# Kernel tuning notes

Hardware: AMD Instinct MI355X
Metric: run time of the kernel (lower is better)

The kernel has to match this reference:

```python
import jax, jax.numpy as jnp
import numpy as np

B, T, D = 2, 2048, 1024
NH, NKV, HD = 16, 4, 64
KD = NKV * HD          # 256
PD = 16                # rope partial dim (rotated dims)
RANK = 8
ALPHA = 1.0
ROPE_BASE = 10000.0


def setup_inputs() -> dict:
    key = jax.random.key(0)
    ks = jax.random.split(key, 10)
    s = 0.02
    return {
        "x":      jax.random.normal(ks[0], (B, T, D), jnp.float32),
        "Wq":     jax.random.normal(ks[1], (D, D), jnp.float32) * s,
        "Wk":     jax.random.normal(ks[2], (KD, D), jnp.float32) * s,
        "Wv":     jax.random.normal(ks[3], (KD, D), jnp.float32) * s,
        "Wproj":  jax.random.normal(ks[4], (D, D), jnp.float32) * s,
        "q_gain": jnp.full((NH,), 5.25, jnp.float32),
        "Aq":     jax.random.normal(ks[5], (RANK, D), jnp.float32) * s,
        "Bq":     jax.random.normal(ks[6], (D, RANK), jnp.float32) * s,
        "Av":     jax.random.normal(ks[7], (RANK, D), jnp.float32) * s,
        "Bv":     jax.random.normal(ks[8], (KD, RANK), jnp.float32) * s,
    }


def _rms_norm(x):
    # F.rms_norm with no weight: x / sqrt(mean(x^2) + eps), eps = dtype machine eps
    eps = jnp.finfo(x.dtype).eps
    return x * jax.lax.rsqrt(jnp.mean(x * x, axis=-1, keepdims=True) + eps)


def _rope_partial(x, cos, sin, pd):
    # x: [B, T, H, HD]; rotate first pd dims (half/half), pass rest through
    h = pd // 2
    x1, x2, rest = x[..., :h], x[..., h:pd], x[..., pd:]
    c = cos[None, :, None, :]  # [1, T, 1, h]
    s = sin[None, :, None, :]
    return jnp.concatenate([x1 * c + x2 * s, -x2 * c + x1 * s, rest], axis=-1)


def reference(x, Wq, Wk, Wv, Wproj, q_gain, Aq, Bq, Av, Bv):
    # projections + per-step LoRA on Q and V (output = alpha * B(A(x)))
    q = x @ Wq.T + ALPHA * ((x @ Aq.T) @ Bq.T)          # [B,T,D]
    k = x @ Wk.T                                        # [B,T,KD]
    v = x @ Wv.T + ALPHA * ((x @ Av.T) @ Bv.T)          # [B,T,KD]

    q = _rms_norm(q.reshape(B, T, NH, HD))
    k = _rms_norm(k.reshape(B, T, NKV, HD))
    v = v.reshape(B, T, NKV, HD)

    # partial RoPE tables: [T, PD//2]
    inv = 1.0 / (ROPE_BASE ** (jnp.arange(0, PD, 2, dtype=jnp.float32) / PD))
    freqs = jnp.arange(T, dtype=jnp.float32)[:, None] * inv[None, :]
    cos, sin = jnp.cos(freqs), jnp.sin(freqs)
    q = _rope_partial(q, cos, sin, PD)
    k = _rope_partial(k, cos, sin, PD)

    # learned per-head QK gain on queries
    q = q * q_gain[None, None, :, None]

    # GQA: repeat-interleave kv heads to NH
    g = NH // NKV
    kf = jnp.repeat(k, g, axis=2)  # [B,T,NH,HD]
    vf = jnp.repeat(v, g, axis=2)

    scale = 1.0 / np.float32(np.sqrt(HD))
    scores = jnp.einsum('bqhd,bkhd->bhqk', q, kf) * scale  # [B,NH,T,T]
    causal = jnp.tril(jnp.ones((T, T), bool))
    scores = jnp.where(causal[None, None], scores, -jnp.inf)
    p = jax.nn.softmax(scores, axis=-1)
    y = jnp.einsum('bhqk,bkhd->bqhd', p, vf).reshape(B, T, D)
    return y @ Wproj.T
```

## Files before the change

### kernel.cpp

```cpp
#include <hip/hip_runtime.h>

#define Tn   2048
#define Dn   1024
#define KDn  256
#define NHn  16
#define NKVn 4
#define Rn   4096

typedef short bf16x8 __attribute__((ext_vector_type(8)));
typedef float f32x4  __attribute__((ext_vector_type(4)));
typedef const __attribute__((address_space(1))) unsigned* gas_p;
typedef __attribute__((address_space(3))) unsigned* las_p;

__device__ unsigned short g_q[(size_t)Rn * Dn];
__device__ unsigned short g_k[(size_t)Rn * KDn];
__device__ unsigned short g_vt[(size_t)2 * NKVn * 64 * Tn];
__device__ unsigned short g_y[(size_t)Rn * Dn];
__device__ unsigned short g_xb[(size_t)Rn * Dn];
__device__ unsigned short g_wq[(size_t)Dn * Dn];
__device__ unsigned short g_wk[(size_t)KDn * Dn];
__device__ unsigned short g_wv[(size_t)KDn * Dn];
__device__ unsigned short g_wp[(size_t)Dn * Dn];
__device__ float g_tq[Rn * 8];
__device__ float g_tv[Rn * 8];

static __device__ __forceinline__ float bf2f(unsigned short u) {
    return __uint_as_float(((unsigned)u) << 16);
}
static __device__ __forceinline__ unsigned short f2bf(float f) {
    unsigned u = __float_as_uint(f);
    u += 0x7fffu + ((u >> 16) & 1u);
    return (unsigned short)(u >> 16);
}
static __device__ __forceinline__ unsigned pk2bf(float a, float b) {
    return (unsigned)f2bf(a) | ((unsigned)f2bf(b) << 16);
}
static __device__ __forceinline__ unsigned cvtpk(float a, float b) {
    unsigned r;
    asm("v_cvt_pk_bf16_f32 %0, %1, %2" : "=v"(r) : "v"(a), "v"(b));
    return r;
}
static __device__ __forceinline__ float wave_sum(float s) {
    #pragma unroll
    for (int off = 32; off; off >>= 1) s += __shfl_xor(s, off);
    return s;
}

__global__ __launch_bounds__(256)
void lora_tmp(const float* __restrict__ x,
              const float* __restrict__ Aq,
              const float* __restrict__ Av) {
    int tid = threadIdx.x, wave = tid >> 6, lane = tid & 63;
    int row = blockIdx.x * 4 + wave;
    const float2* xr = (const float2*)(x + (size_t)row * Dn);
    unsigned* xbo = (unsigned*)g_xb + (size_t)row * (Dn / 2);
    float aq[8], av[8];
    #pragma unroll
    for (int r = 0; r < 8; r++) { aq[r] = 0.f; av[r] = 0.f; }
    for (int it = 0; it < Dn / 128; it++) {
        int j = it * 64 + lane;
        float2 xv = xr[j];
        xbo[j] = pk2bf(xv.x, xv.y);
        #pragma unroll
        for (int r = 0; r < 8; r++) {
            float2 a2 = ((const float2*)(Aq + (size_t)r * Dn))[j];
            aq[r] += xv.x * a2.x + xv.y * a2.y;
        }
        #pragma unroll
        for (int r = 0; r < 8; r++) {
            float2 a2 = ((const float2*)(Av + (size_t)r * Dn))[j];
            av[r] += xv.x * a2.x + xv.y * a2.y;
        }
    }
    #pragma unroll
    for (int r = 0; r < 8; r++) { aq[r] = wave_sum(aq[r]); av[r] = wave_sum(av[r]); }
    if (lane == 0) {
        #pragma unroll
        for (int r = 0; r < 8; r++) { g_tq[row * 8 + r] = aq[r]; g_tv[row * 8 + r] = av[r]; }
    }
}

#define NQ4 (Dn * Dn / 4)
#define NK4 (KDn * Dn / 4)
__global__ __launch_bounds__(256)
void cast_w(const float* __restrict__ Wq, const float* __restrict__ Wk,
            const float* __restrict__ Wv, const float* __restrict__ Wp) {
    int i = blockIdx.x * 256 + threadIdx.x;
    const float* src; unsigned short* dst; int o;
    if      (i < NQ4)                 { src = Wq; dst = g_wq; o = i; }
    else if (i < NQ4 + NK4)           { src = Wk; dst = g_wk; o = i - NQ4; }
    else if (i < NQ4 + 2 * NK4)       { src = Wv; dst = g_wv; o = i - NQ4 - NK4; }
    else                              { src = Wp; dst = g_wp; o = i - NQ4 - 2 * NK4; }
    float4 v = ((const float4*)src)[o];
    ((uint2*)dst)[o] = make_uint2(pk2bf(v.x, v.y), pk2bf(v.z, v.w));
}

template<int MODE>
__global__ __launch_bounds__(256, 2)
void gemm_bt(float* __restrict__ Cout, const float* __restrict__ BqL,
             const float* __restrict__ BvL, const float* __restrict__ qgain,
             int M, int K) {
    const unsigned short* A = (MODE == 0) ? g_xb : g_y;
    int n0 = blockIdx.x * 64, m0 = blockIdx.y * 128;
    const unsigned short* W;
    int wroff, region;
    if (MODE == 0) {
        if (n0 < 1024)      { W = g_wq; wroff = n0;        region = 0; }
        else if (n0 < 1280) { W = g_wk; wroff = n0 - 1024; region = 1; }
        else                { W = g_wv; wroff = n0 - 1280; region = 2; }
    } else { W = g_wp; wroff = n0; region = 3; }

    __shared__ __align__(16) unsigned short SM[12288];
    int tid = threadIdx.x;
    int w = tid >> 6, lane = tid & 63;
    int m_ = lane & 15, quad = lane >> 4;

    int lrow = lane >> 2, lseg = (lane & 3) * 8;
    const unsigned short* agp0 = A + (size_t)(m0 + w * 32 + lrow) * K + lseg;
    const unsigned short* agp1 = A + (size_t)(m0 + w * 32 + 16 + lrow) * K + lseg;
    const unsigned short* wgp  = W + (size_t)(wroff + w * 16 + lrow) * K + lseg;
    int albase0 = (w * 32) * 32;
    int albase1 = (w * 32 + 16) * 32;
    int wlbase  = 8192 + (w * 16) * 32;

    f32x4 acc[2][4];
    #pragma unroll
    for (int im = 0; im < 2; im++)
        #pragma unroll
        for (int in = 0; in < 4; in++) acc[im][in] = (f32x4){0.f, 0.f, 0.f, 0.f};

    __builtin_amdgcn_global_load_lds((gas_p)agp0, (las_p)&SM[albase0], 16, 0, 0);
    __builtin_amdgcn_global_load_lds((gas_p)agp1, (las_p)&SM[albase1], 16, 0, 0);
    __builtin_amdgcn_global_load_lds((gas_p)wgp,  (las_p)&SM[wlbase],  16, 0, 0);

    int nk = K / 32;
    for (int kt = 0; kt < nk; kt++) {
        __syncthreads();
        int cur = kt & 1, nxt = cur ^ 1;
        if (kt + 1 < nk) {
            int ko = (kt + 1) * 32;
            __builtin_amdgcn_global_load_lds((gas_p)(agp0 + ko), (las_p)&SM[nxt * 4096 + albase0], 16, 0, 0);
            __builtin_amdgcn_global_load_lds((gas_p)(agp1 + ko), (las_p)&SM[nxt * 4096 + albase1], 16, 0, 0);
            __builtin_amdgcn_global_load_lds((gas_p)(wgp  + ko), (las_p)&SM[wlbase + nxt * 2048], 16, 0, 0);
        }
        bf16x8 bf[4];
        #pragma unroll
        for (int in = 0; in < 4; in++)
            bf[in] = *(const bf16x8*)&SM[8192 + cur * 2048 + (in * 16 + m_) * 32 + quad * 8];
        #pragma unroll
        for (int im = 0; im < 2; im++) {
            bf16x8 af = *(const bf16x8*)&SM[cur * 4096 + (w * 32 + im * 16 + m_) * 32 + quad * 8];
            #pragma unroll
            for (int in = 0; in < 4; in++)
                acc[im][in] = __builtin_amdgcn_mfma_f32_16x16x32_bf16(af, bf[in], acc[im][in], 0, 0, 0);
        }
    }

    if (MODE == 1) {
        #pragma unroll
        for (int im = 0; im < 2; im++)
            #pragma unroll
            for (int r = 0; r < 4; r++) {
                int row = m0 + w * 32 + im * 16 + quad * 4 + r;
                #pragma unroll
                for (int in = 0; in < 4; in++)
                    Cout[(size_t)row * Dn + (n0 + in * 16 + m_)] = acc[im][in][r];
            }
        return;
    }

    if (region <= 1) {
        float blc[4][8];
        if (region == 0) {
            #pragma unroll
            for (int in = 0; in < 4; in++) {
                const float* bp = BqL + (size_t)(n0 + in * 16 + m_) * 8;
                #pragma unroll
                for (int j = 0; j < 8; j++) blc[in][j] = bp[j];
            }
        }
        float ghead = (region == 0) ? qgain[n0 >> 6] * 0.18033688011112042f : 1.0f;
        #pragma unroll
        for (int im = 0; im < 2; im++) {
            #pragma unroll
            for (int r = 0; r < 4; r++) {
                int row = m0 + w * 32 + im * 16 + quad * 4 + r;
                float vv[4];
                float ss = 0.f;
                if (region == 0) {
                    const float* tp = g_tq + (size_t)row * 8;
                    float tv8[8];
                    #pragma unroll
                    for (int j = 0; j < 8; j++) tv8[j] = tp[j];
                    #pragma unroll
                    for (int in = 0; in < 4; in++) {
                        float val = acc[im][in][r];
                        #pragma unroll
                        for (int j = 0; j < 8; j++) val += tv8[j] * blc[in][j];
                        vv[in] = val; ss += val * val;
                    }
                } else {
                    #pragma unroll
                    for (int in = 0; in < 4; in++) { vv[in] = acc[im][in][r]; ss += vv[in] * vv[in]; }
                }
                ss += __shfl_xor(ss, 1); ss += __shfl_xor(ss, 2);
                ss += __shfl_xor(ss, 4); ss += __shfl_xor(ss, 8);
                float rs = rsqrtf(ss * (1.0f / 64.0f) + 1.1920929e-7f);
                #pragma unroll
                for (int in = 0; in < 4; in++) vv[in] *= rs;
                float p = __shfl_xor(vv[0], 8);
                int t = row & (Tn - 1);
                float fr = (float)t * exp2f(-(float)(m_ & 7) * 1.6609640474436813f);
                float c = cosf(fr), sn = sinf(fr);
                if (m_ < 16) vv[0] = (m_ < 8) ? vv[0] * c + p * sn : p * sn - vv[0] * c;
                #pragma unroll
                for (int in = 0; in < 4; in++) {
                    float val = vv[in] * ghead;
                    int col = n0 + in * 16 + m_;
                    if (region == 0) g_q[(size_t)row * Dn + col] = f2bf(val);
                    else             g_k[(size_t)row * KDn + (col - 1024)] = f2bf(val);
                }
            }
        }
    } else {
        float blc[4][8];
        #pragma unroll
        for (int in = 0; in < 4; in++) {
            const float* bp = BvL + (size_t)(n0 - 1280 + in * 16 + m_) * 8;
            #pragma unroll
            for (int j = 0; j < 8; j++) blc[in][j] = bp[j];
        }
        __syncthreads();
        #pragma unroll
        for (int im = 0; im < 2; im++) {
            #pragma unroll
            for (int r = 0; r < 4; r++) {
                int rl = w * 32 + im * 16 + quad * 4 + r;
                const float* tp = g_tv + (size_t)(m0 + rl) * 8;
                float tv8[8];
                #pragma unroll
                for (int j = 0; j < 8; j++) tv8[j] = tp[j];
                #pragma unroll
                for (int in = 0; in < 4; in++) {
                    float val = acc[im][in][r];
                    #pragma unroll
                    for (int j = 0; j < 8; j++) val += tv8[j] * blc[in][j];
                    SM[(in * 16 + m_) * 136 + rl] = f2bf(val);
                }
            }
        }
        __syncthreads();
        int d = tid >> 2, tseg = (tid & 3) * 32;
        int bb = m0 >> 11, t0 = m0 & (Tn - 1);
        int kvh = (n0 - 1280) >> 6;
        unsigned short* dst = g_vt + (((size_t)(bb * NKVn + kvh) * 64) + d) * Tn + t0 + tseg;
        const uint4* srcv = (const uint4*)&SM[d * 136 + tseg];
        uint4 c0 = srcv[0], c1 = srcv[1], c2 = srcv[2], c3 = srcv[3];
        ((uint4*)dst)[0] = c0; ((uint4*)dst)[1] = c1;
        ((uint4*)dst)[2] = c2; ((uint4*)dst)[3] = c3;
    }
}

__global__ __launch_bounds__(256, 4)
void attn_kernel() {
    __shared__ __align__(16) unsigned short KS[64 * 72];
    __shared__ __align__(16) unsigned short VS[64 * 72];
    __shared__ __align__(16) unsigned short Pt[4][16 * 72];
    int tid = threadIdx.x;
    int w = tid >> 6, lane = tid & 63;
    int q_ = lane & 15, quad = lane >> 4;
    int b = blockIdx.z, kvh = blockIdx.y, h = kvh * 4 + w;
    int bx = blockIdx.x;
    if ((kvh >> 1) & 1) bx = 127 - bx;
    int qb = bx * 16;
    int qg = qb + q_;

    const unsigned short* qrow =
        g_q + ((size_t)(b * Tn + qg) * NHn + h) * 64 + quad * 8;
    bf16x8 Qf0 = *(const bf16x8*)qrow;
    bf16x8 Qf1 = *(const bf16x8*)(qrow + 32);

    int srow = tid >> 2, sseg = (tid & 3) * 16;
    const unsigned short* kgp =
        g_k + ((size_t)(b * Tn + srow) * NKVn + kvh) * 64 + sseg;
    const unsigned short* vgp =
        g_vt + ((size_t)(b * NKVn + kvh) * 64 + srow) * Tn + sseg;

    f32x4 accO[4];
    #pragma unroll
    for (int i = 0; i < 4; i++) accO[i] = (f32x4){0.f, 0.f, 0.f, 0.f};
    float lsum = 0.f;
    int ntiles = (qb + 79) >> 6;

    {
        uint4 ka = *(const uint4*)kgp, kb = *(const uint4*)(kgp + 8);
        uint4 va = *(const uint4*)vgp, vb = *(const uint4*)(vgp + 8);
        *(uint4*)&KS[srow * 72 + sseg] = ka;
        *(uint4*)&KS[srow * 72 + sseg + 8] = kb;
        *(uint4*)&VS[srow * 72 + sseg] = va;
        *(uint4*)&VS[srow * 72 + sseg + 8] = vb;
    }
    __syncthreads();

    for (int kt = 0; kt < ntiles; kt++) {
        bool pre = (kt + 1 < ntiles);
        uint4 kan, kbn, van, vbn;
        if (pre) {
            const unsigned short* kp = kgp + (size_t)(kt + 1) * (64 * NKVn * 64);
            const unsigned short* vp = vgp + (kt + 1) * 64;
            kan = *(const uint4*)kp; kbn = *(const uint4*)(kp + 8);
            van = *(const uint4*)vp; vbn = *(const uint4*)(vp + 8);
        }

        f32x4 s[4];
        __builtin_amdgcn_s_setprio(1);
        #pragma unroll
        for (int ss = 0; ss < 4; ss++) {
            bf16x8 ka = *(const bf16x8*)&KS[(ss * 16 + q_) * 72 + quad * 8];
            bf16x8 kb = *(const bf16x8*)&KS[(ss * 16 + q_) * 72 + 32 + quad * 8];
            s[ss] = (f32x4){0.f, 0.f, 0.f, 0.f};
            s[ss] = __builtin_amdgcn_mfma_f32_16x16x32_bf16(ka, Qf0, s[ss], 0, 0, 0);
            s[ss] = __builtin_amdgcn_mfma_f32_16x16x32_bf16(kb, Qf1, s[ss], 0, 0, 0);
        }
        __builtin_amdgcn_s_setprio(0);

        if (kt == ntiles - 1) {
            #pragma unroll
            for (int ss = 0; ss < 4; ss++) {
                int k0 = kt * 64 + ss * 16 + quad * 4;
                #pragma unroll
                for (int r = 0; r < 4; r++)
                    if (k0 + r > qg) s[ss][r] = -1e30f;
            }
        }
        float p[4][4];
        #pragma unroll
        for (int ss = 0; ss < 4; ss++)
            #pragma unroll
            for (int r = 0; r < 4; r++) {
                p[ss][r] = exp2f(s[ss][r]);
                lsum += p[ss][r];
            }

        unsigned short* pb = &Pt[w][0];
        #pragma unroll
        for (int ss = 0; ss < 4; ss++)
            *(uint2*)&pb[q_ * 72 + ss * 16 + quad * 4] =
                make_uint2(cvtpk(p[ss][0], p[ss][1]), cvtpk(p[ss][2], p[ss][3]));
        bf16x8 pf0 = *(const bf16x8*)&pb[q_ * 72 + quad * 8];
        bf16x8 pf1 = *(const bf16x8*)&pb[q_ * 72 + 32 + quad * 8];

        __builtin_amdgcn_s_setprio(1);
        #pragma unroll
        for (int c = 0; c < 4; c++) {
            bf16x8 vf0 = *(const bf16x8*)&VS[(c * 16 + q_) * 72 + quad * 8];
            bf16x8 vf1 = *(const bf16x8*)&VS[(c * 16 + q_) * 72 + 32 + quad * 8];
            accO[c] = __builtin_amdgcn_mfma_f32_16x16x32_bf16(vf0, pf0, accO[c], 0, 0, 0);
            accO[c] = __builtin_amdgcn_mfma_f32_16x16x32_bf16(vf1, pf1, accO[c], 0, 0, 0);
        }
        __builtin_amdgcn_s_setprio(0);

        __syncthreads();
        if (pre) {
            *(uint4*)&KS[srow * 72 + sseg] = kan;
            *(uint4*)&KS[srow * 72 + sseg + 8] = kbn;
            *(uint4*)&VS[srow * 72 + sseg] = van;
            *(uint4*)&VS[srow * 72 + sseg + 8] = vbn;
        }
        __syncthreads();
    }

    lsum += __shfl_xor(lsum, 16);
    lsum += __shfl_xor(lsum, 32);
    float invl = 1.0f / lsum;
    unsigned short* yp = g_y + ((size_t)(b * Tn + qg) * NHn + h) * 64;
    #pragma unroll
    for (int c = 0; c < 4; c++) {
        uint2 o = make_uint2(cvtpk(accO[c][0] * invl, accO[c][1] * invl),
                             cvtpk(accO[c][2] * invl, accO[c][3] * invl));
        *(uint2*)&yp[c * 16 + quad * 4] = o;
    }
}

extern "C" void kernel_launch(void* const* d_in, const int* in_sizes, int n_in,
                              void* d_out, int out_size, void* d_ws, size_t ws_size,
                              hipStream_t stream) {
    const float* x  = (const float*)d_in[0];
    const float* Wq = (const float*)d_in[1];
    const float* Wk = (const float*)d_in[2];
    const float* Wv = (const float*)d_in[3];
    const float* Wp = (const float*)d_in[4];
    const float* qg = (const float*)d_in[5];
    const float* Aq = (const float*)d_in[6];
    const float* Bq = (const float*)d_in[7];
    const float* Av = (const float*)d_in[8];
    const float* Bv = (const float*)d_in[9];
    float* out = (float*)d_out;

    lora_tmp<<<dim3(Rn / 4), dim3(256), 0, stream>>>(x, Aq, Av);
    cast_w<<<dim3((NQ4 * 2 + NK4 * 2) / 256), dim3(256), 0, stream>>>(Wq, Wk, Wv, Wp);
    gemm_bt<0><<<dim3(1536 / 64, Rn / 128), dim3(256), 0, stream>>>(
        nullptr, Bq, Bv, qg, Rn, Dn);
    attn_kernel<<<dim3(Tn / 16, NKVn, 2), dim3(256), 0, stream>>>();
    gemm_bt<1><<<dim3(Dn / 64, Rn / 128), dim3(256), 0, stream>>>(
        out, nullptr, nullptr, nullptr, Rn, Dn);
}
```

Before: 221.0 us.

## Double GEMM K-tile to 64 and remap blocks across XCDs

The bf16 GEMM kernel now stages 64-wide K tiles instead of 32, which halves the number of barriers and main-loop iterations and gives each sync twice as many MFMAs. Shared memory doubles to 48KB per block. A block-index swizzle also spreads contiguous tiles round-robin over 8 groups, apparently to match the XCD chiplet layout for better L2 locality. The catches are higher LDS use, which may limit the 2-blocks-per-CU occupancy, and possible bank conflicts from the 128-byte row stride.

```diff
diff --git a/kernel.cpp b/kernel.cpp
--- a/kernel.cpp
+++ b/kernel.cpp
@@ -101,7 +101,13 @@
              const float* __restrict__ BvL, const float* __restrict__ qgain,
              int M, int K) {
     const unsigned short* A = (MODE == 0) ? g_xb : g_y;
-    int n0 = blockIdx.x * 64, m0 = blockIdx.y * 128;
+
+    int gx = gridDim.x;
+    int flat = blockIdx.y * gx + blockIdx.x;
+    int cpx = (gx * gridDim.y) >> 3;
+    int flat2 = (flat & 7) * cpx + (flat >> 3);
+    int n0 = (flat2 % gx) * 64, m0 = (flat2 / gx) * 128;
+
     const unsigned short* W;
     int wroff, region;
     if (MODE == 0) {
@@ -110,18 +116,25 @@
         else                { W = g_wv; wroff = n0 - 1280; region = 2; }
     } else { W = g_wp; wroff = n0; region = 3; }
 
-    __shared__ __align__(16) unsigned short SM[12288];
+    __shared__ __align__(16) unsigned short SM[24576];
     int tid = threadIdx.x;
     int w = tid >> 6, lane = tid & 63;
     int m_ = lane & 15, quad = lane >> 4;
 
-    int lrow = lane >> 2, lseg = (lane & 3) * 8;
-    const unsigned short* agp0 = A + (size_t)(m0 + w * 32 + lrow) * K + lseg;
-    const unsigned short* agp1 = A + (size_t)(m0 + w * 32 + 16 + lrow) * K + lseg;
-    const unsigned short* wgp  = W + (size_t)(wroff + w * 16 + lrow) * K + lseg;
-    int albase0 = (w * 32) * 32;
-    int albase1 = (w * 32 + 16) * 32;
-    int wlbase  = 8192 + (w * 16) * 32;
+    int lrow = lane >> 3, lseg = (lane & 7) * 8;
+    const unsigned short* agp[4];
+    #pragma unroll
+    for (int i = 0; i < 4; i++)
+        agp[i] = A + (size_t)(m0 + w * 32 + i * 8 + lrow) * K + lseg;
+    const unsigned short* wgp[2];
+    #pragma unroll
+    for (int i = 0; i < 2; i++)
+        wgp[i] = W + (size_t)(wroff + w * 16 + i * 8 + lrow) * K + lseg;
+    int alb[4], wlb[2];
+    #pragma unroll
+    for (int i = 0; i < 4; i++) alb[i] = (w * 32 + i * 8) * 64;
+    #pragma unroll
+    for (int i = 0; i < 2; i++) wlb[i] = 16384 + (w * 16 + i * 8) * 64;
 
     f32x4 acc[2][4];
     #pragma unroll
@@ -129,30 +142,43 @@
         #pragma unroll
         for (int in = 0; in < 4; in++) acc[im][in] = (f32x4){0.f, 0.f, 0.f, 0.f};
 
-    __builtin_amdgcn_global_load_lds((gas_p)agp0, (las_p)&SM[albase0], 16, 0, 0);
-    __builtin_amdgcn_global_load_lds((gas_p)agp1, (las_p)&SM[albase1], 16, 0, 0);
-    __builtin_amdgcn_global_load_lds((gas_p)wgp,  (las_p)&SM[wlbase],  16, 0, 0);
-
-    int nk = K / 32;
+    #pragma unroll
+    for (int i = 0; i < 4; i++)
+        __builtin_amdgcn_global_load_lds((gas_p)agp[i], (las_p)&SM[alb[i]], 16, 0, 0);
+    #pragma unroll
+    for (int i = 0; i < 2; i++)
+        __builtin_amdgcn_global_load_lds((gas_p)wgp[i], (las_p)&SM[wlb[i]], 16, 0, 0);
+
+    int nk = K >> 6;
     for (int kt = 0; kt < nk; kt++) {
         __syncthreads();
         int cur = kt & 1, nxt = cur ^ 1;
         if (kt + 1 < nk) {
-            int ko = (kt + 1) * 32;
-            __builtin_amdgcn_global_load_lds((gas_p)(agp0 + ko), (las_p)&SM[nxt * 4096 + albase0], 16, 0, 0);
-            __builtin_amdgcn_global_load_lds((gas_p)(agp1 + ko), (las_p)&SM[nxt * 4096 + albase1], 16, 0, 0);
-            __builtin_amdgcn_global_load_lds((gas_p)(wgp  + ko), (las_p)&SM[wlbase + nxt * 2048], 16, 0, 0);
-        }
-        bf16x8 bf[4];
-        #pragma unroll
-        for (int in = 0; in < 4; in++)
-            bf[in] = *(const bf16x8*)&SM[8192 + cur * 2048 + (in * 16 + m_) * 32 + quad * 8];
-        #pragma unroll
-        for (int im = 0; im < 2; im++) {
-            bf16x8 af = *(const bf16x8*)&SM[cur * 4096 + (w * 32 + im * 16 + m_) * 32 + quad * 8];
+            int ko = (kt + 1) * 64;
+            #pragma unroll
+            for (int i = 0; i < 4; i++)
+                __builtin_amdgcn_global_load_lds((gas_p)(agp[i] + ko),
+                    (las_p)&SM[nxt * 8192 + alb[i]], 16, 0, 0);
+            #pragma unroll
+            for (int i = 0; i < 2; i++)
+                __builtin_amdgcn_global_load_lds((gas_p)(wgp[i] + ko),
+                    (las_p)&SM[nxt * 4096 + wlb[i]], 16, 0, 0);
+        }
+        #pragma unroll
+        for (int kk = 0; kk < 2; kk++) {
+            bf16x8 bf[4];
             #pragma unroll
             for (int in = 0; in < 4; in++)
-                acc[im][in] = __builtin_amdgcn_mfma_f32_16x16x32_bf16(af, bf[in], acc[im][in], 0, 0, 0);
+                bf[in] = *(const bf16x8*)&SM[16384 + cur * 4096 +
+                                             (in * 16 + m_) * 64 + kk * 32 + quad * 8];
+            #pragma unroll
+            for (int im = 0; im < 2; im++) {
+                bf16x8 af = *(const bf16x8*)&SM[cur * 8192 +
+                                                (w * 32 + im * 16 + m_) * 64 + kk * 32 + quad * 8];
+                #pragma unroll
+                for (int in = 0; in < 4; in++)
+                    acc[im][in] = __builtin_amdgcn_mfma_f32_16x16x32_bf16(af, bf[in], acc[im][in], 0, 0, 0);
+            }
         }
     }
 
```

Result: faster. 195.6 us (-11.5%).
